# Optimization experiments

Hardware: AMD Instinct MI355X
Metric: run time of the kernel (lower is better)

## Reference

```python
import jax, jax.numpy as jnp
import numpy as np

NUM_Q = 100000; NUM_C = 1000; D = 128; BS = 128; SEQ = 128
QN = 4; CN = 10; NQC = 4; AGG_HOPS = 2; RANK_K = 10
NEG = jnp.float32(-1e9)


def setup_inputs() -> dict:
    key = jax.random.key(0)
    ks = iter(jax.random.split(key, 40))
    def nrm(shape, scale=0.05):
        return jax.random.normal(next(ks), shape, dtype=jnp.float32) * scale
    inp = {}
    inp['question_seq'] = jax.random.randint(next(ks), (BS, SEQ), 0, NUM_Q, dtype=jnp.int32)
    inp['correct_seq'] = jax.random.randint(next(ks), (BS, SEQ), 0, 2, dtype=jnp.int32)
    inp['mask_seq'] = jnp.ones((BS, SEQ), dtype=jnp.int32)
    inp['question_neighbors'] = jax.random.randint(next(ks), (NUM_Q, QN), 0, NUM_C, dtype=jnp.int32)
    inp['concept_neighbors'] = jax.random.randint(next(ks), (NUM_C, CN), 0, NUM_Q, dtype=jnp.int32)
    inp['qc_table'] = jax.random.randint(next(ks), (NUM_Q, NQC), 0, NUM_C, dtype=jnp.int32)
    inp['Eq'] = nrm((NUM_Q, D), 1.0)
    inp['Ec'] = nrm((NUM_C, D), 1.0)
    inp['Er'] = nrm((2, D), 1.0)
    inp['W_ih1'] = nrm((3 * D, 2 * D)); inp['W_hh1'] = nrm((3 * D, D))
    inp['b_ih1'] = nrm((3 * D,)); inp['b_hh1'] = nrm((3 * D,))
    inp['W_ih2'] = nrm((3 * D, D)); inp['W_hh2'] = nrm((3 * D, D))
    inp['b_ih2'] = nrm((3 * D,)); inp['b_hh2'] = nrm((3 * D,))
    inp['W_agg'] = nrm((AGG_HOPS, D, D)); inp['b_agg'] = nrm((AGG_HOPS, D))
    inp['W_agg_last'] = nrm((D, D)); inp['b_agg_last'] = nrm((D,))
    inp['Wq'] = nrm((D, D)); inp['bq'] = nrm((D,))
    inp['Wk'] = nrm((D, D)); inp['bk'] = nrm((D,))
    inp['Ww'] = nrm((1, 2 * D)); inp['bw'] = nrm((1,))
    inp['h1_init'] = nrm((BS, D)); inp['h2_init'] = nrm((BS, D))
    return inp


def _gru(x, h, W_ih, W_hh, b_ih, b_hh):
    gi = x @ W_ih.T + b_ih
    gh = h @ W_hh.T + b_hh
    ir, iz, i_n = jnp.split(gi, 3, axis=-1)
    hr, hz, hn = jnp.split(gh, 3, axis=-1)
    r = jax.nn.sigmoid(ir + hr)
    z = jax.nn.sigmoid(iz + hz)
    n = jnp.tanh(i_n + r * hn)
    return (1 - z) * n + z * h


def _forward(question_seq, correct_seq, mask_seq, question_neighbors, concept_neighbors, qc_table,
             Eq, Ec, Er, W_ih1, W_hh1, b_ih1, b_hh1, W_ih2, W_hh2, b_ih2, b_hh2,
             W_agg, b_agg, W_agg_last, b_agg_last, Wq, bq, Wk, bk, Ww, bw, h1_init, h2_init):
    bs, seq_len = question_seq.shape
    d = Eq.shape[1]
    # detached question embeddings of the whole history (recap scoring key)
    K_all = jax.lax.stop_gradient(Eq[question_seq])  # [bs, seq, d]
    Wh, Wqc = Ww[:, :d], Ww[:, d:]  # MLP_W split over [state; question_concept]

    def predict(qc, hist, hist_mask):
        # qc: [bs,nqc,d], hist: [bs,ns,d], hist_mask: [bs,ns]
        Kp = qc @ Wk.T + bk                     # MLP_key
        Qp = hist @ Wq.T + bq                   # MLP_query
        logits = jnp.einsum('bsd,bqd->bsq', Qp, Kp)
        logits = jnp.where(hist_mask[:, :, None], logits, NEG)
        w = jax.nn.softmax(logits.reshape(bs, -1), axis=1)
        # pairwise sigmoid(MLP_W([h; e])) without materializing the concat
        v = jax.nn.sigmoid((hist @ Wh[0])[:, :, None] + (qc @ Wqc[0])[:, None, :] + bw[0])
        return jnp.sum(w * v.reshape(bs, -1), axis=1)

    def step(carry, t):
        h1, h2, state_hist, y_hat = carry
        q_t = jnp.take(question_seq, t, axis=1)
        r_t = jnp.take(correct_seq, t, axis=1)
        m_t = jnp.take(mask_seq, t, axis=1) != 0
        # --- 2-hop GNN aggregation (question -> concept -> question) ---
        n1 = question_neighbors[q_t]            # [bs, QN] concept ids
        n2 = concept_neighbors[n1]              # [bs, QN, CN] question ids
        emb = [Eq[q_t], Ec[n1], Eq[n2]]
        for i in range(AGG_HOPS):
            for j in range(AGG_HOPS - i):
                s = jnp.mean(emb[j + 1], axis=-2) + emb[j]
                emb[j] = jnp.tanh(s @ W_agg[j].T + b_agg[j])
        agg = jnp.tanh(emb[0] @ W_agg_last.T + b_agg_last)
        emb_q = jnp.where(m_t[:, None], agg, Eq[q_t])
        # --- GRU state updates (dropout in eval mode = identity) ---
        h1n = _gru(jnp.concatenate([emb_q, Er[r_t]], axis=1), h1, W_ih1, W_hh1, b_ih1, b_hh1)
        g2 = _gru(h1n, h2, W_ih2, W_hh2, b_ih2, b_hh2)
        # --- next question + its concepts ---
        q_next = jnp.take(question_seq, t + 1, axis=1)
        qc = jnp.concatenate([Eq[q_next][:, None], Ec[qc_table[q_next]]], axis=1)  # [bs, 1+NQC, d]
        # --- soft recap: top-k history states by detached embedding similarity ---
        scores = jnp.einsum('bsd,bd->bs', K_all, jax.lax.stop_gradient(Eq[q_next]))
        valid = jnp.arange(seq_len) < t
        scores = jnp.where(valid[None, :], scores, NEG)
        top_vals, top_idx = jax.lax.top_k(scores, RANK_K)
        sel = jnp.take_along_axis(state_hist, top_idx[:, :, None], axis=1)  # [bs, k, d]
        sel_mask = top_vals > NEG / 2
        hist = jnp.concatenate([g2[:, None], sel], axis=1)
        hist_mask = jnp.concatenate([jnp.ones((bs, 1), dtype=bool), sel_mask], axis=1)
        p = predict(qc, hist, hist_mask)
        idx = jnp.where(t == 0, 0, t + 1)  # original writes y_hat[:,0] at t==0
        y_hat = y_hat.at[:, idx].set(p)
        # h2 / state_history NOT updated at t==0 (original `continue`)
        upd = t > 0
        h2n = jnp.where(upd, g2, h2)
        state_hist = jnp.where(upd, state_hist.at[:, t].set(g2), state_hist)
        return (h1n, h2n, state_hist, y_hat), None

    init = (h1_init, h2_init,
            jnp.zeros((bs, seq_len, d), jnp.float32),
            jnp.zeros((bs, seq_len), jnp.float32))
    (_, _, _, y_hat), _ = jax.lax.scan(jax.checkpoint(step), init, jnp.arange(seq_len - 1))
    return y_hat


def reference(question_seq, correct_seq, mask_seq, question_neighbors, concept_neighbors, qc_table,
              Eq, Ec, Er, W_ih1, W_hh1, b_ih1, b_hh1, W_ih2, W_hh2, b_ih2, b_hh2,
              W_agg, b_agg, W_agg_last, b_agg_last, Wq, bq, Wk, bk, Ww, bw, h1_init, h2_init):
    return _forward(question_seq, correct_seq, mask_seq, question_neighbors, concept_neighbors, qc_table,
                    Eq, Ec, Er, W_ih1, W_hh1, b_ih1, b_hh1, W_ih2, W_hh2, b_ih2, b_hh2,
                    W_agg, b_agg, W_agg_last, b_agg_last, Wq, bq, Wk, bk, Ww, bw, h1_init, h2_init)
```

## Files before the change

kernel.cpp:

```cpp
#include <hip/hip_runtime.h>

#define DD 128
#define BSZ 128
#define SEQL 128
#define TST 127
#define QNN 4
#define CNN 10
#define NQCC 4
#define RKK 10
#define NEGV -1000000000.0f

#define OFF_WTA0    0
#define OFF_WTA1    16384
#define OFF_WTAL    32768
#define OFF_WTIH1A  49152
#define OFF_ERIH1   98304
#define OFF_MT      99072
#define OFF_WPACK   115456
#define OFF_ECA0    189184
#define OFF_E1C     317184
#define OFF_KQC     445184
#define OFF_VQCC    509184
#define OFF_KBC     510184
#define OFF_U       511184
#define OFF_W2      511312
#define OFF_C0      511440
#define OFF_GRAM    511488
#define OFF_GI1     511488
#define OFF_KQ0     6753792
#define OFF_VQC0    7802368
#define OFF_KB0     7818752
#define OFF_TIX     7835136
#define OFF_TMSK    7997696
#define OFF_CID     8160256

typedef __fp16 h2 __attribute__((ext_vector_type(2)));

__device__ __forceinline__ float sigm(float x) { return 1.0f / (1.0f + __expf(-x)); }
__device__ __forceinline__ unsigned pkh(float a, float b) {
  h2 v; v.x = (__fp16)a; v.y = (__fp16)b;
  return __builtin_bit_cast(unsigned, v);
}
__device__ __forceinline__ float fd2(float acc, unsigned w, h2 x) {
  return __builtin_amdgcn_fdot2(__builtin_bit_cast(h2, w), x, acc, false);
}
__device__ __forceinline__ float fd2u(float acc, unsigned w, unsigned x) {
  return __builtin_amdgcn_fdot2(__builtin_bit_cast(h2, w), __builtin_bit_cast(h2, x), acc, false);
}

__global__ __launch_bounds__(256) void k_prep(
    const float* __restrict__ W_hh1, const float* __restrict__ W_ih2,
    const float* __restrict__ W_hh2, const float* __restrict__ W_agg,
    const float* __restrict__ W_agg_last, const float* __restrict__ W_ih1,
    const float* __restrict__ Er, float* __restrict__ ws) {
  int idx = blockIdx.x * 256 + threadIdx.x;
  const int TOT = 172800;
  for (int o = idx; o < TOT; o += gridDim.x * 256) {
    int r = o;
    if (r < 16384) { int j = r >> 7, i = r & 127; ws[OFF_WTA0 + r] = W_agg[i * 128 + j]; continue; }
    r -= 16384;
    if (r < 16384) { int j = r >> 7, i = r & 127; ws[OFF_WTA1 + r] = W_agg[16384 + i * 128 + j]; continue; }
    r -= 16384;
    if (r < 16384) { int j = r >> 7, i = r & 127; ws[OFF_WTAL + r] = W_agg_last[i * 128 + j]; continue; }
    r -= 16384;
    if (r < 49152) { int j = r / 384, i = r % 384; ws[OFF_WTIH1A + r] = W_ih1[i * 256 + j]; continue; }
    r -= 49152;
    if (r < 768) {
      int rr = r / 384, i2 = r % 384;
      float a = 0.f;
      for (int j = 0; j < 128; ++j) a += Er[rr * 128 + j] * W_ih1[i2 * 256 + 128 + j];
      ws[OFF_ERIH1 + r] = a; continue;
    }
    r -= 768;
    {
      int n = r & 3; int q = r >> 2;
      int i = q & 127; q >>= 7;
      int kk = q & 3; q >>= 2;
      int jc = q & 3; int c = q >> 2;
      int j0 = jc * 32 + kk * 8 + n * 2;
      const float* row;
      if (c < 3) row = W_hh1 + (size_t)(c * 128 + i) * 128;
      else if (c < 6) row = W_ih2 + (size_t)((c - 3) * 128 + i) * 128;
      else row = W_hh2 + (size_t)((c - 6) * 128 + i) * 128;
      ((unsigned*)ws)[OFF_WPACK + r] = pkh(row[j0], row[j0 + 1]);
    }
  }
}

__global__ __launch_bounds__(128) void k_mqk(
    const float* __restrict__ Wq, const float* __restrict__ Wk,
    const float* __restrict__ bq, const float* __restrict__ bk,
    float* __restrict__ ws) {
  int j = blockIdx.x;
  int tid = threadIdx.x;
  if (j < 128) {
    __shared__ float wkc[128];
    wkc[tid] = Wk[tid * 128 + j];
    __syncthreads();
    float a = 0.f;
    for (int l = 0; l < 128; ++l) a = fmaf(Wq[l * 128 + tid], wkc[l], a);
    ws[OFF_MT + j * 128 + tid] = a;
  } else if (j == 128) {
    float a = 0.f;
    for (int l = 0; l < 128; ++l) a = fmaf(Wq[l * 128 + tid], bk[l], a);
    ws[OFF_U + tid] = a;
  } else {
    float a = 0.f;
    for (int l = 0; l < 128; ++l) a = fmaf(bq[l], Wk[l * 128 + tid], a);
    ws[OFF_W2 + tid] = a;
    __shared__ float sc[128];
    sc[tid] = bq[tid] * bk[tid];
    __syncthreads();
    if (tid == 0) { float s = 0.f; for (int l = 0; l < 128; ++l) s += sc[l]; ws[OFF_C0] = s; }
  }
}

__global__ __launch_bounds__(128) void k_concept(
    const int* __restrict__ cnbr, const float* __restrict__ Eq,
    const float* __restrict__ Ec, const float* __restrict__ b_agg,
    const float* __restrict__ Ww, float* __restrict__ ws) {
  int c = blockIdx.x;
  int tid = threadIdx.x;
  __shared__ int s_nb[CNN];
  __shared__ float s_v[DD], s_ec[DD], s_t2[DD], s_w2[DD], s_kb2[DD];
  if (tid < CNN) s_nb[tid] = cnbr[c * CNN + tid];
  __syncthreads();
  float ec = Ec[c * DD + tid];
  float cm = 0.f;
#pragma unroll
  for (int l = 0; l < CNN; ++l) cm += Eq[(size_t)s_nb[l] * DD + tid];
  s_ec[tid] = ec;
  s_v[tid] = cm * 0.1f + ec;
  __syncthreads();
  const float* WtA0 = ws + OFF_WTA0;
  const float* WtA1 = ws + OFF_WTA1;
  const float* MT = ws + OFF_MT;
  float a1 = 0.f, a0 = 0.f, kq = 0.f;
#pragma unroll 8
  for (int j = 0; j < DD; ++j) {
    a1 += WtA1[j * DD + tid] * s_v[j];
    a0 += WtA0[j * DD + tid] * s_ec[j];
    kq += MT[j * DD + tid] * s_ec[j];
  }
  ws[OFF_E1C + c * DD + tid] = tanhf(a1 + b_agg[DD + tid]);
  ws[OFF_ECA0 + c * DD + tid] = a0;
  s_t2[tid] = kq + ws[OFF_U + tid];
  s_w2[tid] = s_ec[tid] * Ww[128 + tid];
  s_kb2[tid] = s_ec[tid] * ws[OFF_W2 + tid];
  __syncthreads();
  if (tid < 64) {
    ((unsigned*)ws)[OFF_KQC + c * 64 + tid] = pkh(s_t2[2 * tid], s_t2[2 * tid + 1]);
    float pa = s_w2[tid] + s_w2[tid + 64];
    float pb = s_kb2[tid] + s_kb2[tid + 64];
    for (int off = 32; off > 0; off >>= 1) { pa += __shfl_down(pa, off); pb += __shfl_down(pb, off); }
    if (tid == 0) { ws[OFF_VQCC + c] = pa; ws[OFF_KBC + c] = pb + ws[OFF_C0]; }
  }
}

__global__ __launch_bounds__(256) void k_gram(
    const int* __restrict__ qseq, const float* __restrict__ Eq,
    const float* __restrict__ Ww, float* __restrict__ ws) {
  int b = blockIdx.x;
  int tid = threadIdx.x;
  __shared__ float sX[128][129];
  __shared__ float s_tmp[2][8][DD];
  __shared__ int sq[SEQL];
  __shared__ float sU[DD], sWqc[DD], sW2[DD];
  if (tid < 128) {
    sq[tid] = qseq[b * SEQL + tid];
    sU[tid] = ws[OFF_U + tid];
    sWqc[tid] = Ww[128 + tid];
    sW2[tid] = ws[OFF_W2 + tid];
  }
  __syncthreads();
  for (int o = tid; o < 128 * 32; o += 256) {
    int s = o >> 5, p = o & 31;
    float4 v = ((const float4*)(Eq + (size_t)sq[s] * DD))[p];
    sX[s][p * 4] = v.x; sX[s][p * 4 + 1] = v.y; sX[s][p * 4 + 2] = v.z; sX[s][p * 4 + 3] = v.w;
  }
  __syncthreads();
  {
    int r0 = (tid >> 4) * 8, c0 = (tid & 15) * 8;
    float acc[8][8];
#pragma unroll
    for (int u = 0; u < 8; ++u)
#pragma unroll
      for (int v = 0; v < 8; ++v) acc[u][v] = 0.f;
    for (int k = 0; k < 128; ++k) {
      float a[8], bb[8];
#pragma unroll
      for (int u = 0; u < 8; ++u) { a[u] = sX[r0 + u][k]; bb[u] = sX[c0 + u][k]; }
#pragma unroll
      for (int u = 0; u < 8; ++u)
#pragma unroll
        for (int v = 0; v < 8; ++v) acc[u][v] = fmaf(a[u], bb[v], acc[u][v]);
    }
    float* gb = ws + OFF_GRAM + (size_t)b * 16384;
#pragma unroll
    for (int u = 0; u < 8; ++u) {
      float4 v0 = {acc[u][0], acc[u][1], acc[u][2], acc[u][3]};
      float4 v1 = {acc[u][4], acc[u][5], acc[u][6], acc[u][7]};
      ((float4*)(gb + (size_t)(r0 + u) * 128 + c0))[0] = v0;
      ((float4*)(gb + (size_t)(r0 + u) * 128 + c0 + 4))[0] = v1;
    }
  }
  {
    const float* MT = ws + OFF_MT;
    unsigned* KQ0 = (unsigned*)ws + OFF_KQ0;
    int i = tid & 127, half = tid >> 7;
    int s0 = half * 64;
    for (int sb = 0; sb < 64; sb += 8) {
      float acc[8];
#pragma unroll
      for (int u = 0; u < 8; ++u) acc[u] = 0.f;
      for (int j = 0; j < DD; ++j) {
        float w = MT[j * DD + i];
#pragma unroll
        for (int u = 0; u < 8; ++u) acc[u] = fmaf(w, sX[s0 + sb + u][j], acc[u]);
      }
      __syncthreads();
#pragma unroll
      for (int u = 0; u < 8; ++u) s_tmp[half][u][i] = acc[u] + sU[i];
      __syncthreads();
      for (int o = tid; o < 16 * 64; o += 256) {
        int rr = o >> 6, e = o & 63;
        int hh = rr >> 3, uu = rr & 7;
        int s = hh * 64 + sb + uu;
        KQ0[((size_t)b * 128 + s) * 64 + e] = pkh(s_tmp[hh][uu][2 * e], s_tmp[hh][uu][2 * e + 1]);
      }
      __syncthreads();
    }
  }
  if (tid < 128) {
    float a = 0.f, kb = 0.f;
    for (int j = 0; j < DD; ++j) {
      float xv = sX[tid][j];
      a = fmaf(xv, sWqc[j], a);
      kb = fmaf(xv, sW2[j], kb);
    }
    ws[OFF_VQC0 + b * 128 + tid] = a;
    ws[OFF_KB0 + b * 128 + tid] = kb + ws[OFF_C0];
  }
}

__global__ __launch_bounds__(128) void k_topk(
    const int* __restrict__ qseq, const int* __restrict__ qctab,
    float* __restrict__ ws) {
  int* tix = (int*)(ws + OFF_TIX);
  int* tmsk = (int*)(ws + OFF_TMSK);
  int* cid = (int*)(ws + OFF_CID);
  int tid = threadIdx.x;
  int lane = tid & 63, wv = tid >> 6;
  int bt = blockIdx.x * 2 + wv;
  int b = bt / TST, t = bt - b * TST;
  if (lane < 5) {
    int qn = qseq[b * SEQL + t + 1];
    cid[(b * 128 + t + 1) * 5 + lane] = (lane == 0) ? qn : qctab[qn * NQCC + lane - 1];
  }
  const float* grow = ws + OFF_GRAM + ((size_t)b * 128 + (t + 1)) * 128;
  float v0 = (lane < t) ? grow[lane] : NEGV;
  float v1 = (lane + 64 < t) ? grow[lane + 64] : NEGV;
  for (int k = 0; k < RKK; ++k) {
    float bv = v0; int bi = lane;
    if (v1 > bv) { bv = v1; bi = lane + 64; }
    for (int off = 32; off > 0; off >>= 1) {
      float ov = __shfl_down(bv, off);
      int oi = __shfl_down(bi, off);
      if (ov > bv || (ov == bv && oi < bi)) { bv = ov; bi = oi; }
    }
    bv = __shfl(bv, 0); bi = __shfl(bi, 0);
    if (lane == 0) {
      tix[bt * RKK + k] = bi;
      tmsk[bt * RKK + k] = (bv > NEGV * 0.5f) ? 1 : 0;
    }
    if (bi == lane) v0 = -__builtin_inff();
    if (bi == lane + 64) v1 = -__builtin_inff();
  }
}

__global__ __launch_bounds__(128) void k_agg(
    const int* __restrict__ qseq, const int* __restrict__ rseq,
    const int* __restrict__ mseq, const int* __restrict__ qnbr,
    const float* __restrict__ Eq, const float* __restrict__ b_agg,
    const float* __restrict__ b_agg_last, const float* __restrict__ b_ih1,
    float* __restrict__ ws) {
  int blk = blockIdx.x;
  int b = blk >> 4, g = blk & 15;
  int t0 = g * 8;
  int nu = (t0 + 8 <= TST) ? 8 : (TST - t0);
  int tid = threadIdx.x;
  __shared__ float s_a[8][DD], s_b[8][DD], s_c[8][DD];
  __shared__ int s_q[8], s_r[8], s_m[8];
  __shared__ int s_n1[8][QNN];
  if (tid < 8) {
    int ok = tid < nu;
    int idx = b * SEQL + (ok ? (t0 + tid) : 0);
    s_q[tid] = qseq[idx];
    s_r[tid] = ok ? rseq[idx] : 0;
    s_m[tid] = ok ? mseq[idx] : 0;
  }
  __syncthreads();
  if (tid < 32) { int u = tid >> 2, k = tid & 3; s_n1[u][k] = qnbr[s_q[u] * QNN + k]; }
  for (int o = tid; o < 8 * 32; o += 128) {
    int u = o >> 5, p = o & 31;
    float4 v = ((const float4*)(Eq + (size_t)s_q[u] * DD))[p];
    s_a[u][p * 4] = v.x; s_a[u][p * 4 + 1] = v.y; s_a[u][p * 4 + 2] = v.z; s_a[u][p * 4 + 3] = v.w;
  }
  __syncthreads();
  const float* WtA0 = ws + OFF_WTA0;
  const float* WtAL = ws + OFF_WTAL;
  const float* WtIH1A = ws + OFF_WTIH1A;
  const float* EcA0 = ws + OFF_ECA0;
  const float* E1C = ws + OFF_E1C;
  float acc[8];
#pragma unroll
  for (int u = 0; u < 8; ++u) acc[u] = 0.f;
  for (int j = 0; j < DD; ++j) {
    float w = WtA0[j * DD + tid];
#pragma unroll
    for (int u = 0; u < 8; ++u) acc[u] = fmaf(w, s_a[u][j], acc[u]);
  }
  float bat = b_agg[tid];
#pragma unroll
  for (int u = 0; u < 8; ++u) {
    int n0 = s_n1[u][0], n1 = s_n1[u][1], n2 = s_n1[u][2], n3 = s_n1[u][3];
    float pre0 = 0.25f * (EcA0[n0 * DD + tid] + EcA0[n1 * DD + tid] + EcA0[n2 * DD + tid] + EcA0[n3 * DD + tid]);
    float e0 = tanhf(acc[u] + pre0 + bat);
    float e1m = 0.25f * (E1C[n0 * DD + tid] + E1C[n1 * DD + tid] + E1C[n2 * DD + tid] + E1C[n3 * DD + tid]);
    s_b[u][tid] = e1m + e0;
  }
  __syncthreads();
#pragma unroll
  for (int u = 0; u < 8; ++u) acc[u] = 0.f;
  for (int j = 0; j < DD; ++j) {
    float w = WtA0[j * DD + tid];
#pragma unroll
    for (int u = 0; u < 8; ++u) acc[u] = fmaf(w, s_b[u][j], acc[u]);
  }
#pragma unroll
  for (int u = 0; u < 8; ++u) s_c[u][tid] = tanhf(acc[u] + bat);
  __syncthreads();
#pragma unroll
  for (int u = 0; u < 8; ++u) acc[u] = 0.f;
  for (int j = 0; j < DD; ++j) {
    float w = WtAL[j * DD + tid];
#pragma unroll
    for (int u = 0; u < 8; ++u) acc[u] = fmaf(w, s_c[u][j], acc[u]);
  }
  float balt = b_agg_last[tid];
#pragma unroll
  for (int u = 0; u < 8; ++u) {
    float aggv = tanhf(acc[u] + balt);
    s_b[u][tid] = s_m[u] ? aggv : s_a[u][tid];
  }
  __syncthreads();
  float g0[8], g1[8], g2[8];
#pragma unroll
  for (int u = 0; u < 8; ++u) { g0[u] = 0.f; g1[u] = 0.f; g2[u] = 0.f; }
  for (int j = 0; j < DD; ++j) {
    float w0 = WtIH1A[j * 384 + tid];
    float w1 = WtIH1A[j * 384 + 128 + tid];
    float w2 = WtIH1A[j * 384 + 256 + tid];
#pragma unroll
    for (int u = 0; u < 8; ++u) {
      float x = s_b[u][j];
      g0[u] = fmaf(w0, x, g0[u]);
      g1[u] = fmaf(w1, x, g1[u]);
      g2[u] = fmaf(w2, x, g2[u]);
    }
  }
  for (int u = 0; u < nu; ++u) {
    const float* ErI = ws + OFF_ERIH1 + s_r[u] * 384;
    float* gi1 = ws + OFF_GI1 + (size_t)(b * TST + t0 + u) * 384;
    gi1[tid] = g0[u] + ErI[tid] + b_ih1[tid];
    gi1[128 + tid] = g1[u] + ErI[128 + tid] + b_ih1[128 + tid];
    gi1[256 + tid] = g2[u] + ErI[256 + tid] + b_ih1[256 + tid];
  }
}

__global__ __launch_bounds__(512, 2) void k_seq(
    const float* __restrict__ b_hh1, const float* __restrict__ b_ih2,
    const float* __restrict__ b_hh2, const float* __restrict__ Ww,
    const float* __restrict__ bw, const float* __restrict__ h1i,
    const float* __restrict__ h2i, float* __restrict__ ws,
    float* __restrict__ out) {
  const int tid = threadIdx.x;
  const int b = blockIdx.x;
  const int i = tid >> 2, jc = tid & 3;
  const int lane = tid & 63, wv = tid >> 6;
  const int bt0 = b * TST;

  const float4* gi1f4 = (const float4*)(ws + OFF_GI1);
  const unsigned* KQ0 = (const unsigned*)ws + OFF_KQ0;
  const unsigned* KQC = (const unsigned*)ws + OFF_KQC;
  const float* vqc0_all = ws + OFF_VQC0;
  const float* vqcC_all = ws + OFF_VQCC;
  const float* kb0_all = ws + OFF_KB0;
  const float* kbC_all = ws + OFF_KBC;
  const int* tix_all = (const int*)(ws + OFF_TIX);
  const int* tmsk_all = (const int*)(ws + OFF_TMSK);
  const int* cid_all = (const int*)(ws + OFF_CID);
  const uint4* wp = (const uint4*)((const unsigned*)ws + OFF_WPACK);

  __shared__ float s_h1[DD], s_h2[DD], s_h1n[DD], s_g2[DD];
  __shared__ unsigned qph_pk[SEQL * 64 + 10240];
  __shared__ unsigned s_Kq[5 * 66];
  __shared__ float s_gi1[384];
  __shared__ float s_vhh[SEQL];
  __shared__ float s_logit[64];
  __shared__ float s_bhh1[384], s_bih2[384], s_bhh2[384];
  __shared__ float s_vh[11], s_vqc[2][5], s_kb[2][5], s_bw;
  __shared__ int s_tix[RKK], s_hm[11], s_cidn[5];

  uint4 wgt[9][4];
#pragma unroll
  for (int c = 0; c < 9; ++c)
#pragma unroll
    for (int kk = 0; kk < 4; ++kk)
      wgt[c][kk] = wp[((c * 4 + jc) * 4 + kk) * 128 + i];
#pragma unroll
  for (int c = 0; c < 9; ++c)
#pragma unroll
    for (int kk = 0; kk < 4; ++kk)
      asm volatile("" : "+v"(wgt[c][kk].x), "+v"(wgt[c][kk].y),
                        "+v"(wgt[c][kk].z), "+v"(wgt[c][kk].w));

  if (tid < 384) { s_bhh1[tid] = b_hh1[tid]; s_bih2[tid] = b_ih2[tid]; s_bhh2[tid] = b_hh2[tid]; }
  if (tid < 128) { s_h1[tid] = h1i[b * DD + tid]; s_h2[tid] = h2i[b * DD + tid]; s_vhh[tid] = 0.f; }
  if (tid >= 55 && tid < 64) s_logit[tid] = NEGV;
  float wh_lo = 0.f, wh_hi = 0.f;
  if (wv == 7) { wh_lo = Ww[lane]; wh_hi = Ww[64 + lane]; }
  if (tid == 0) { s_bw = bw[0]; out[b * SEQL + 1] = 0.f; s_hm[0] = 1; }
  if (tid >= 296 && tid < 301) s_cidn[tid - 296] = cid_all[(b * 128 + 1) * 5 + tid - 296];
  if (tid >= 304 && tid < 314) s_tix[tid - 304] = tix_all[bt0 * RKK + tid - 304];
  if (tid >= 320 && tid < 330) s_hm[1 + tid - 320] = tmsk_all[bt0 * RKK + tid - 320];
  __syncthreads();
  for (int o = tid; o < SEQL * 64; o += 512) qph_pk[o] = 0u;
  if (tid < 96) ((float4*)s_gi1)[tid] = gi1f4[(size_t)bt0 * 96 + tid];
  else if (tid < 256) {
    int kx = tid - 96;
    { int s = kx >> 6, e = kx & 63;
      s_Kq[s * 66 + e] = (s == 0) ? KQ0[(size_t)(b * 128 + 1) * 64 + e] : KQC[s_cidn[s] * 64 + e]; }
    { int kx2 = kx + 160; int s = kx2 >> 6, e = kx2 & 63;
      s_Kq[s * 66 + e] = KQC[s_cidn[s] * 64 + e]; }
  } else if (tid < 266) {
    int k = tid - 256;
    if (k < 5) s_vqc[0][k] = (k == 0) ? vqc0_all[b * 128 + 1] : vqcC_all[s_cidn[k]];
    else { int s = k - 5; s_kb[0][s] = (s == 0) ? kb0_all[b * 128 + 1] : kbC_all[s_cidn[s]]; }
  }
  __syncthreads();
  if (tid < 5) s_cidn[tid] = cid_all[(b * 128 + 2) * 5 + tid];
  __syncthreads();

  for (int t = 0; t < TST; ++t) {
    const int par = t & 1, parn = par ^ 1;
    const int tpn = (t + 1 < TST) ? t + 1 : TST - 1;
    const int tpp = (t + 2 < TST) ? t + 2 : TST - 1;
    float4 pf4 = {0.f, 0.f, 0.f, 0.f};
    unsigned pfu = 0, pfu2 = 0; int pfs = 0; float pfv = 0.f, pfkb = 0.f;

    if (tid < 96) pf4 = gi1f4[(size_t)(bt0 + tpn) * 96 + tid];
    else if (tid < 256) {
      int kx = tid - 96;
      { int s = kx >> 6, e = kx & 63;
        pfu = (s == 0) ? KQ0[(size_t)(b * 128 + tpn + 1) * 64 + e] : KQC[s_cidn[s] * 64 + e]; }
      { int kx2 = kx + 160; int s = kx2 >> 6, e = kx2 & 63;
        pfu2 = KQC[s_cidn[s] * 64 + e]; }
    } else if (tid < 291) {
      int k = tid - 256;
      if (k < 5) pfv = (k == 0) ? vqc0_all[b * 128 + tpn + 1] : vqcC_all[s_cidn[k]];
      else if (k < 10) { int s = k - 5; pfkb = (s == 0) ? kb0_all[b * 128 + tpn + 1] : kbC_all[s_cidn[s]]; }
      else if (k < 20) pfs = tix_all[(bt0 + tpn) * RKK + k - 10];
      else if (k < 30) pfs = tmsk_all[(bt0 + tpn) * RKK + k - 20];
      else pfs = cid_all[(b * 128 + tpp + 1) * 5 + k - 30];
    }
    {
      const float4* xp = (const float4*)s_h1 + (jc << 3);
      float a0 = 0.f, a1 = 0.f, a2 = 0.f;
#pragma unroll
      for (int kk = 0; kk < 4; ++kk) {
        float4 x0 = xp[2 * kk], x1 = xp[2 * kk + 1];
        h2 p0 = __builtin_amdgcn_cvt_pkrtz(x0.x, x0.y);
        h2 p1 = __builtin_amdgcn_cvt_pkrtz(x0.z, x0.w);
        h2 p2 = __builtin_amdgcn_cvt_pkrtz(x1.x, x1.y);
        h2 p3 = __builtin_amdgcn_cvt_pkrtz(x1.z, x1.w);
        uint4 w;
        w = wgt[0][kk]; a0 = fd2(a0, w.x, p0); a0 = fd2(a0, w.y, p1); a0 = fd2(a0, w.z, p2); a0 = fd2(a0, w.w, p3);
        w = wgt[1][kk]; a1 = fd2(a1, w.x, p0); a1 = fd2(a1, w.y, p1); a1 = fd2(a1, w.z, p2); a1 = fd2(a1, w.w, p3);
        w = wgt[2][kk]; a2 = fd2(a2, w.x, p0); a2 = fd2(a2, w.y, p1); a2 = fd2(a2, w.z, p2); a2 = fd2(a2, w.w, p3);
      }
      a0 += __shfl_down(a0, 2); a0 += __shfl_down(a0, 1);
      a1 += __shfl_down(a1, 2); a1 += __shfl_down(a1, 1);
      a2 += __shfl_down(a2, 2); a2 += __shfl_down(a2, 1);
      if (jc == 0) {
        float r = sigm(s_gi1[i] + a0 + s_bhh1[i]);
        float z = sigm(s_gi1[128 + i] + a1 + s_bhh1[128 + i]);
        float n = tanhf(s_gi1[256 + i] + r * (a2 + s_bhh1[256 + i]));
        s_h1n[i] = (1.f - z) * n + z * s_h1[i];
      }
    }
    __syncthreads();

    {
      const float4* xn = (const float4*)s_h1n + (jc << 3);
      const float4* xh = (const float4*)s_h2 + (jc << 3);
      float a0 = 0.f, a1 = 0.f, a2 = 0.f, c0 = 0.f, c1 = 0.f, c2 = 0.f;
#pragma unroll
      for (int kk = 0; kk < 4; ++kk) {
        float4 n0 = xn[2 * kk], n1 = xn[2 * kk + 1];
        h2 p0 = __builtin_amdgcn_cvt_pkrtz(n0.x, n0.y);
        h2 p1 = __builtin_amdgcn_cvt_pkrtz(n0.z, n0.w);
        h2 p2 = __builtin_amdgcn_cvt_pkrtz(n1.x, n1.y);
        h2 p3 = __builtin_amdgcn_cvt_pkrtz(n1.z, n1.w);
        float4 h0 = xh[2 * kk], h1v = xh[2 * kk + 1];
        h2 q0 = __builtin_amdgcn_cvt_pkrtz(h0.x, h0.y);
        h2 q1 = __builtin_amdgcn_cvt_pkrtz(h0.z, h0.w);
        h2 q2 = __builtin_amdgcn_cvt_pkrtz(h1v.x, h1v.y);
        h2 q3 = __builtin_amdgcn_cvt_pkrtz(h1v.z, h1v.w);
        uint4 w;
        w = wgt[3][kk]; a0 = fd2(a0, w.x, p0); a0 = fd2(a0, w.y, p1); a0 = fd2(a0, w.z, p2); a0 = fd2(a0, w.w, p3);
        w = wgt[4][kk]; a1 = fd2(a1, w.x, p0); a1 = fd2(a1, w.y, p1); a1 = fd2(a1, w.z, p2); a1 = fd2(a1, w.w, p3);
        w = wgt[5][kk]; a2 = fd2(a2, w.x, p0); a2 = fd2(a2, w.y, p1); a2 = fd2(a2, w.z, p2); a2 = fd2(a2, w.w, p3);
        w = wgt[6][kk]; c0 = fd2(c0, w.x, q0); c0 = fd2(c0, w.y, q1); c0 = fd2(c0, w.z, q2); c0 = fd2(c0, w.w, q3);
        w = wgt[7][kk]; c1 = fd2(c1, w.x, q0); c1 = fd2(c1, w.y, q1); c1 = fd2(c1, w.z, q2); c1 = fd2(c1, w.w, q3);
        w = wgt[8][kk]; c2 = fd2(c2, w.x, q0); c2 = fd2(c2, w.y, q1); c2 = fd2(c2, w.z, q2); c2 = fd2(c2, w.w, q3);
      }
      a0 += __shfl_down(a0, 2); a0 += __shfl_down(a0, 1);
      a1 += __shfl_down(a1, 2); a1 += __shfl_down(a1, 1);
      a2 += __shfl_down(a2, 2); a2 += __shfl_down(a2, 1);
      c0 += __shfl_down(c0, 2); c0 += __shfl_down(c0, 1);
      c1 += __shfl_down(c1, 2); c1 += __shfl_down(c1, 1);
      c2 += __shfl_down(c2, 2); c2 += __shfl_down(c2, 1);
      if (jc == 0) {
        float r = sigm(a0 + s_bih2[i] + c0 + s_bhh2[i]);
        float z = sigm(a1 + s_bih2[128 + i] + c1 + s_bhh2[128 + i]);
        float n = tanhf(a2 + s_bih2[256 + i] + r * (c2 + s_bhh2[256 + i]));
        s_g2[i] = (1.f - z) * n + z * s_h2[i];
      }
    }
    __syncthreads();

    if (tid < 440) {
      int p = tid >> 3, sub = tid & 7;
      int q = p / 5, s = p - q * 5;
      const unsigned* kpr = &s_Kq[s * 66 + sub * 8];
      float a = 0.f;
      if (q == 0) {
        const float* gp = s_g2 + sub * 16;
#pragma unroll
        for (int k = 0; k < 8; ++k) {
          h2 x = __builtin_amdgcn_cvt_pkrtz(gp[2 * k], gp[2 * k + 1]);
          a = fd2(a, kpr[k], x);
        }
      } else {
        int row = s_tix[q - 1];
        int xr = row & 63;
        const unsigned* ro = qph_pk + row * 64;
#pragma unroll
        for (int k = 0; k < 8; ++k) a = fd2u(a, ro[(sub * 8 + k) ^ xr], kpr[k]);
      }
      a += __shfl_down(a, 4);
      a += __shfl_down(a, 2);
      a += __shfl_down(a, 1);
      if (sub == 0) s_logit[p] = s_hm[q] ? (a + s_kb[par][s]) : NEGV;
    } else if (wv == 7) {
      float pa = s_g2[lane] * wh_lo + s_g2[64 + lane] * wh_hi;
      for (int off = 32; off > 0; off >>= 1) pa += __shfl_down(pa, off);
      if (lane == 0) s_vh[0] = pa;
      if (lane >= 16 && lane < 26) s_vh[1 + lane - 16] = s_vhh[s_tix[lane - 16]];
    }
    __syncthreads();

    if (wv == 7) {
      float l = s_logit[lane];
      float m = l;
      for (int off = 32; off > 0; off >>= 1) m = fmaxf(m, __shfl_xor(m, off));
      float e = __expf(l - m);
      float v = 0.f;
      if (lane < 55) {
        int q = lane / 5, s = lane - q * 5;
        v = sigm(s_vh[q] + s_vqc[par][s] + s_bw);
      }
      float num = e * v, den = e;
      for (int off = 32; off > 0; off >>= 1) { num += __shfl_xor(num, off); den += __shfl_xor(den, off); }
      if (lane == 0) out[b * SEQL + ((t == 0) ? 0 : (t + 1))] = num / den;
    } else {
      if (tid < 96) ((float4*)s_gi1)[tid] = pf4;
      else if (tid < 256) {
        int kx = tid - 96;
        { int s = kx >> 6, e = kx & 63; s_Kq[s * 66 + e] = pfu; }
        { int kx2 = kx + 160; int s = kx2 >> 6, e = kx2 & 63; s_Kq[s * 66 + e] = pfu2; }
      } else if (tid < 291) {
        int k = tid - 256;
        if (k < 5) s_vqc[parn][k] = pfv;
        else if (k < 10) s_kb[parn][k - 5] = pfkb;
        else if (k < 20) s_tix[k - 10] = pfs;
        else if (k < 30) s_hm[1 + k - 20] = pfs;
        else s_cidn[k - 30] = pfs;
      }
      if (tid >= 320 && tid < 448) {
        int ii = tid - 320;
        s_h1[ii] = s_h1n[ii];
        if (t > 0) s_h2[ii] = s_g2[ii];
      }
      if (t > 0 && tid >= 96 && tid < 160) {
        int k2 = tid - 96;
        qph_pk[t * 64 + (k2 ^ (t & 63))] = pkh(s_g2[2 * k2], s_g2[2 * k2 + 1]);
      }
      if (tid == 0 && t > 0) s_vhh[t] = s_vh[0];
    }
    __syncthreads();
  }
}

extern "C" void kernel_launch(void* const* d_in, const int* in_sizes, int n_in,
                              void* d_out, int out_size, void* d_ws, size_t ws_size,
                              hipStream_t stream) {
  (void)in_sizes; (void)n_in; (void)out_size; (void)ws_size;
  const int* qseq = (const int*)d_in[0];
  const int* rseq = (const int*)d_in[1];
  const int* mseq = (const int*)d_in[2];
  const int* qnbr = (const int*)d_in[3];
  const int* cnbr = (const int*)d_in[4];
  const int* qctab = (const int*)d_in[5];
  const float* Eq = (const float*)d_in[6];
  const float* Ec = (const float*)d_in[7];
  const float* Er = (const float*)d_in[8];
  const float* W_ih1 = (const float*)d_in[9];
  const float* W_hh1 = (const float*)d_in[10];
  const float* b_ih1 = (const float*)d_in[11];
  const float* b_hh1 = (const float*)d_in[12];
  const float* W_ih2 = (const float*)d_in[13];
  const float* W_hh2 = (const float*)d_in[14];
  const float* b_ih2 = (const float*)d_in[15];
  const float* b_hh2 = (const float*)d_in[16];
  const float* W_agg = (const float*)d_in[17];
  const float* b_agg = (const float*)d_in[18];
  const float* W_agg_last = (const float*)d_in[19];
  const float* b_agg_last = (const float*)d_in[20];
  const float* Wq = (const float*)d_in[21];
  const float* bq = (const float*)d_in[22];
  const float* Wk = (const float*)d_in[23];
  const float* bk = (const float*)d_in[24];
  const float* Ww = (const float*)d_in[25];
  const float* bw = (const float*)d_in[26];
  const float* h1i = (const float*)d_in[27];
  const float* h2i = (const float*)d_in[28];
  float* ws = (float*)d_ws;
  float* out = (float*)d_out;

  hipLaunchKernelGGL(k_prep, dim3(675), dim3(256), 0, stream,
                     W_hh1, W_ih2, W_hh2, W_agg, W_agg_last, W_ih1, Er, ws);
  hipLaunchKernelGGL(k_mqk, dim3(130), dim3(128), 0, stream,
                     Wq, Wk, bq, bk, ws);
  hipLaunchKernelGGL(k_concept, dim3(1000), dim3(128), 0, stream,
                     cnbr, Eq, Ec, b_agg, Ww, ws);
  hipLaunchKernelGGL(k_gram, dim3(BSZ), dim3(256), 0, stream,
                     qseq, Eq, Ww, ws);
  hipLaunchKernelGGL(k_topk, dim3(BSZ * TST / 2), dim3(128), 0, stream,
                     qseq, qctab, ws);
  hipLaunchKernelGGL(k_agg, dim3(BSZ * 16), dim3(128), 0, stream,
                     qseq, rseq, mseq, qnbr, Eq, b_agg, b_agg_last, b_ih1, ws);
  hipLaunchKernelGGL(k_seq, dim3(BSZ), dim3(512), 0, stream,
                     b_hh1, b_ih2, b_hh2, Ww, bw, h1i, h2i, ws, out);
}
```

Baseline: 677.8 us.

## Pad shared state vectors and history rows, use lightweight LDS-only barriers

Pads the h1/h2/g2 shared vectors by inserting 4 floats every 32 elements, so the four jc lanes' float4 reads land in different banks. Replaces the XOR-swizzled history rows with a stride-66 padded layout, which simplifies the index math. Swaps __syncthreads for a custom barrier that waits only on LDS counters (lgkmcnt), so outstanding global prefetch loads no longer stall each step's barriers. The barrier relies on the prefetched values being consumed only after a later wait; any missed dependency would be a correctness risk.

```diff
diff --git a/kernel.cpp b/kernel.cpp
--- a/kernel.cpp
+++ b/kernel.cpp
@@ -34,6 +34,8 @@
 #define OFF_TMSK    7997696
 #define OFF_CID     8160256
 
+#define XI(e) ((e) + (((e) >> 5) << 2))
+
 typedef __fp16 h2 __attribute__((ext_vector_type(2)));
 
 __device__ __forceinline__ float sigm(float x) { return 1.0f / (1.0f + __expf(-x)); }
@@ -46,6 +48,11 @@
 }
 __device__ __forceinline__ float fd2u(float acc, unsigned w, unsigned x) {
   return __builtin_amdgcn_fdot2(__builtin_bit_cast(h2, w), __builtin_bit_cast(h2, x), acc, false);
+}
+__device__ __forceinline__ void bar() {
+  asm volatile("s_waitcnt lgkmcnt(0)" ::: "memory");
+  __builtin_amdgcn_s_barrier();
+  asm volatile("" ::: "memory");
 }
 
 __global__ __launch_bounds__(256) void k_prep(
@@ -402,8 +409,8 @@
   const int* cid_all = (const int*)(ws + OFF_CID);
   const uint4* wp = (const uint4*)((const unsigned*)ws + OFF_WPACK);
 
-  __shared__ float s_h1[DD], s_h2[DD], s_h1n[DD], s_g2[DD];
-  __shared__ unsigned qph_pk[SEQL * 64 + 10240];
+  __shared__ float s_h1[144], s_h2[144], s_h1n[144], s_g2[144];
+  __shared__ unsigned qph_pk[SEQL * 66];
   __shared__ unsigned s_Kq[5 * 66];
   __shared__ float s_gi1[384];
   __shared__ float s_vhh[SEQL];
@@ -426,7 +433,7 @@
                         "+v"(wgt[c][kk].z), "+v"(wgt[c][kk].w));
 
   if (tid < 384) { s_bhh1[tid] = b_hh1[tid]; s_bih2[tid] = b_ih2[tid]; s_bhh2[tid] = b_hh2[tid]; }
-  if (tid < 128) { s_h1[tid] = h1i[b * DD + tid]; s_h2[tid] = h2i[b * DD + tid]; s_vhh[tid] = 0.f; }
+  if (tid < 128) { s_h1[XI(tid)] = h1i[b * DD + tid]; s_h2[XI(tid)] = h2i[b * DD + tid]; s_vhh[tid] = 0.f; }
   if (tid >= 55 && tid < 64) s_logit[tid] = NEGV;
   float wh_lo = 0.f, wh_hi = 0.f;
   if (wv == 7) { wh_lo = Ww[lane]; wh_hi = Ww[64 + lane]; }
@@ -435,7 +442,7 @@
   if (tid >= 304 && tid < 314) s_tix[tid - 304] = tix_all[bt0 * RKK + tid - 304];
   if (tid >= 320 && tid < 330) s_hm[1 + tid - 320] = tmsk_all[bt0 * RKK + tid - 320];
   __syncthreads();
-  for (int o = tid; o < SEQL * 64; o += 512) qph_pk[o] = 0u;
+  for (int o = tid; o < SEQL * 66; o += 512) qph_pk[o] = 0u;
   if (tid < 96) ((float4*)s_gi1)[tid] = gi1f4[(size_t)bt0 * 96 + tid];
   else if (tid < 256) {
     int kx = tid - 96;
@@ -475,7 +482,7 @@
       else pfs = cid_all[(b * 128 + tpp + 1) * 5 + k - 30];
     }
     {
-      const float4* xp = (const float4*)s_h1 + (jc << 3);
+      const float4* xp = (const float4*)s_h1 + jc * 9;
       float a0 = 0.f, a1 = 0.f, a2 = 0.f;
 #pragma unroll
       for (int kk = 0; kk < 4; ++kk) {
@@ -496,14 +503,14 @@
         float r = sigm(s_gi1[i] + a0 + s_bhh1[i]);
         float z = sigm(s_gi1[128 + i] + a1 + s_bhh1[128 + i]);
         float n = tanhf(s_gi1[256 + i] + r * (a2 + s_bhh1[256 + i]));
-        s_h1n[i] = (1.f - z) * n + z * s_h1[i];
-      }
-    }
-    __syncthreads();
+        s_h1n[XI(i)] = (1.f - z) * n + z * s_h1[XI(i)];
+      }
+    }
+    bar();
 
     {
-      const float4* xn = (const float4*)s_h1n + (jc << 3);
-      const float4* xh = (const float4*)s_h2 + (jc << 3);
+      const float4* xn = (const float4*)s_h1n + jc * 9;
+      const float4* xh = (const float4*)s_h2 + jc * 9;
       float a0 = 0.f, a1 = 0.f, a2 = 0.f, c0 = 0.f, c1 = 0.f, c2 = 0.f;
 #pragma unroll
       for (int kk = 0; kk < 4; ++kk) {
@@ -535,10 +542,10 @@
         float r = sigm(a0 + s_bih2[i] + c0 + s_bhh2[i]);
         float z = sigm(a1 + s_bih2[128 + i] + c1 + s_bhh2[128 + i]);
         float n = tanhf(a2 + s_bih2[256 + i] + r * (c2 + s_bhh2[256 + i]));
-        s_g2[i] = (1.f - z) * n + z * s_h2[i];
-      }
-    }
-    __syncthreads();
+        s_g2[XI(i)] = (1.f - z) * n + z * s_h2[XI(i)];
+      }
+    }
+    bar();
 
     if (tid < 440) {
       int p = tid >> 3, sub = tid & 7;
@@ -546,30 +553,29 @@
       const unsigned* kpr = &s_Kq[s * 66 + sub * 8];
       float a = 0.f;
       if (q == 0) {
-        const float* gp = s_g2 + sub * 16;
+        int e0 = sub * 16;
 #pragma unroll
         for (int k = 0; k < 8; ++k) {
-          h2 x = __builtin_amdgcn_cvt_pkrtz(gp[2 * k], gp[2 * k + 1]);
+          int e = XI(e0 + 2 * k);
+          h2 x = __builtin_amdgcn_cvt_pkrtz(s_g2[e], s_g2[e + 1]);
           a = fd2(a, kpr[k], x);
         }
       } else {
-        int row = s_tix[q - 1];
-        int xr = row & 63;
-        const unsigned* ro = qph_pk + row * 64;
-#pragma unroll
-        for (int k = 0; k < 8; ++k) a = fd2u(a, ro[(sub * 8 + k) ^ xr], kpr[k]);
+        const unsigned* ro = qph_pk + s_tix[q - 1] * 66;
+#pragma unroll
+        for (int k = 0; k < 8; ++k) a = fd2u(a, ro[sub * 8 + k], kpr[k]);
       }
       a += __shfl_down(a, 4);
       a += __shfl_down(a, 2);
       a += __shfl_down(a, 1);
       if (sub == 0) s_logit[p] = s_hm[q] ? (a + s_kb[par][s]) : NEGV;
     } else if (wv == 7) {
-      float pa = s_g2[lane] * wh_lo + s_g2[64 + lane] * wh_hi;
+      float pa = s_g2[XI(lane)] * wh_lo + s_g2[XI(64 + lane)] * wh_hi;
       for (int off = 32; off > 0; off >>= 1) pa += __shfl_down(pa, off);
       if (lane == 0) s_vh[0] = pa;
       if (lane >= 16 && lane < 26) s_vh[1 + lane - 16] = s_vhh[s_tix[lane - 16]];
     }
-    __syncthreads();
+    bar();
 
     if (wv == 7) {
       float l = s_logit[lane];
@@ -600,16 +606,17 @@
       }
       if (tid >= 320 && tid < 448) {
         int ii = tid - 320;
-        s_h1[ii] = s_h1n[ii];
-        if (t > 0) s_h2[ii] = s_g2[ii];
+        s_h1[XI(ii)] = s_h1n[XI(ii)];
+        if (t > 0) s_h2[XI(ii)] = s_g2[XI(ii)];
       }
       if (t > 0 && tid >= 96 && tid < 160) {
         int k2 = tid - 96;
-        qph_pk[t * 64 + (k2 ^ (t & 63))] = pkh(s_g2[2 * k2], s_g2[2 * k2 + 1]);
+        int e = XI(2 * k2);
+        qph_pk[t * 66 + k2] = pkh(s_g2[e], s_g2[e + 1]);
       }
       if (tid == 0 && t > 0) s_vhh[t] = s_vh[0];
     }
-    __syncthreads();
+    bar();
   }
 }
 
```

New measurement: 655.6 us. 1.03x faster.
